# Performance work log

Measured on AMD Instinct MI355X. Metric: run time of the kernel, lower is better.

Reference implementation:

```python
import jax, jax.numpy as jnp
import numpy as np

B = 4096        # args.batch_size
M = 2           # n_views (and m in approximate_hsic_zy)
N = B * M       # total rows after torch.cat of views
D = 128         # projector feature dim
GAMMA = 3.0     # args.gamma
SIGMA = 1.0     # Gaussian kernel bandwidth used by compute_gaussian_kernel


def setup_inputs() -> dict:
    key = jax.random.key(0)
    x = jax.random.normal(key, (N, D), dtype=jnp.float32)
    # module applies l2_norm (F.normalize dim=1) before hsic_objective
    feat = x / jnp.maximum(jnp.linalg.norm(x, axis=1, keepdims=True), 1e-12)
    return {"feat": feat}


def _gaussian_kernel(x, y):
    # pairwise squared distances via the GEMM trick, then Gaussian kernel
    sq = (jnp.sum(x * x, axis=1)[:, None]
          + jnp.sum(y * y, axis=1)[None, :]
          - 2.0 * (x @ y.T))
    sq = jnp.maximum(sq, 0.0)
    return jnp.exp(-sq / (2.0 * SIGMA * SIGMA))


def _approximate_hsic_zy(K):
    # labels = cat([arange(B)]*M); labels-equality matrix; exclude diagonal.
    lab = jnp.tile(jnp.arange(B), M)                      # [N]
    eq = (lab[:, None] == lab[None, :]).astype(K.dtype)   # [N,N]
    offdiag = 1.0 - jnp.eye(N, dtype=K.dtype)
    # positives / negatives sums over off-diagonal entries (same math as the
    # boolean-mask view/reshape in torch, expressed as masked reductions)
    pos_sum = jnp.sum(K * eq * offdiag)
    neg_sum = jnp.sum(K * (1.0 - eq) * offdiag)
    term_1 = pos_sum / (B * M * (M - 1))
    term_2 = neg_sum / (B ** 2 * M ** 2)
    term_3 = 1.0 / (M - 1)
    scale = B / (B - 1.0)  # get_label_weights(batch_size) stand-in
    return scale * (term_1 - term_2 - term_3)


def _hsic_regular(K):
    # HSIC(z,z) with doubly-centered kernel: mean(Kc * Kc) since Kx == Ky
    row_m = jnp.mean(K, axis=0, keepdims=True)
    col_m = jnp.mean(K, axis=1, keepdims=True)
    tot_m = jnp.mean(K)
    Kc = K - row_m - col_m + tot_m
    return jnp.mean(Kc * Kc)


def reference(feat):
    K = _gaussian_kernel(feat, feat)          # [N,N] pairwise Gaussian kernel
    hsic_zy = _approximate_hsic_zy(K)
    hsic_zz = _hsic_regular(K)
    return -hsic_zy + GAMMA * jnp.sqrt(hsic_zz)
```

## Files before the change

kernel.cpp:

```cpp
#include <hip/hip_runtime.h>
#include <hip/hip_bf16.h>


using bf16   = __bf16;
using bf16x8 = __attribute__((ext_vector_type(8))) __bf16;
using f32x4  = __attribute__((ext_vector_type(4))) float;

#define N_ROWS 8192
#define LOG2E 1.4426950408889634f

#if __has_builtin(__builtin_amdgcn_exp2f)
#define EXP2(x) __builtin_amdgcn_exp2f(x)
#else
#define EXP2(x) exp2f(x)
#endif

__global__ __launch_bounds__(256) void prep_kernel(
    const float* __restrict__ feat, unsigned short* __restrict__ xb) {
  const int g = blockIdx.x * 256 + threadIdx.x;
  const float4 a = ((const float4*)feat)[g * 2];
  const float4 b = ((const float4*)feat)[g * 2 + 1];
  bf16x8 r;
  r[0] = (__bf16)a.x; r[1] = (__bf16)a.y; r[2] = (__bf16)a.z; r[3] = (__bf16)a.w;
  r[4] = (__bf16)b.x; r[5] = (__bf16)b.y; r[6] = (__bf16)b.z; r[7] = (__bf16)b.w;
  ((bf16x8*)xb)[g] = r;
}

__global__ __launch_bounds__(256, 2) void gram_kernel(
    const bf16* __restrict__ xb, float* __restrict__ rpart,
    float* __restrict__ bscal) {
  const int bjc = blockIdx.x, bi = blockIdx.y;
  const int tid = threadIdx.x, lane = tid & 63, w = tid >> 6;
  const int wr = w >> 1, wc = w & 1;
  const int l15 = lane & 15, l4 = lane >> 4;

  __shared__ char  lds_a[32768];
  __shared__ float rbuf[128];
  __shared__ float sS[4], sD[4], sP[4];

  {
    const int rowbase = bi * 128;
#pragma unroll
    for (int i = 0; i < 8; ++i) {
      const int c = tid + i * 256;
      const int row = c >> 4, seg = c & 15;
      const bf16x8 v = *(const bf16x8*)(xb + (rowbase + row) * 128 + seg * 8);
      const int sw = ((row << 8) | (seg << 4)) ^ ((row & 7) << 4);
      *(bf16x8*)(lds_a + sw) = v;
    }
    if (tid < 128) rbuf[tid] = 0.f;
  }
  __syncthreads();

  float rsum[4][4] = {};
  float s2a = 0.f, s2b = 0.f, pdiag = 0.f, ppos = 0.f;

  bf16x8 bn[4];
  {
    const int brow0 = (bjc * 4) * 128 + wc * 64;
#pragma unroll
    for (int f = 0; f < 4; ++f)
      bn[f] = *(const bf16x8*)(xb + (brow0 + f * 16 + l15) * 128 + l4 * 8);
  }

#pragma unroll
  for (int t = 0; t < 4; ++t) {
    const int bj = bjc * 4 + t;
    const int brow0 = bj * 128 + wc * 64;

    f32x4 acc[4][4];
#pragma unroll
    for (int fr = 0; fr < 4; ++fr)
#pragma unroll
      for (int fc = 0; fc < 4; ++fc)
#pragma unroll
        for (int e = 0; e < 4; ++e) acc[fr][fc][e] = -1.0f;

#pragma unroll
    for (int ks = 0; ks < 4; ++ks) {
      bf16x8 bb[4];
#pragma unroll
      for (int f = 0; f < 4; ++f) bb[f] = bn[f];

      if (ks < 3 || t < 3) {
        const int nks = (ks + 1) & 3;
        const int nbrow0 = (ks < 3) ? brow0 : brow0 + 128;
#pragma unroll
        for (int f = 0; f < 4; ++f)
          bn[f] = *(const bf16x8*)(xb + (nbrow0 + f * 16 + l15) * 128 +
                                   nks * 32 + l4 * 8);
      }

#pragma unroll
      for (int fr = 0; fr < 4; ++fr) {
        const int arow = wr * 64 + fr * 16 + l15;
        const int byte = (arow << 8) + ks * 64 + (l4 << 4);
        const bf16x8 a = *(const bf16x8*)(lds_a + (byte ^ ((arow & 7) << 4)));
#pragma unroll
        for (int fc = 0; fc < 4; ++fc)
          acc[fr][fc] = __builtin_amdgcn_mfma_f32_16x16x32_bf16(
              a, bb[fc], acc[fr][fc], 0, 0, 0);
      }
    }

    const int dt = bj - bi;
    const bool isd = (dt == 0);
    const bool isp = (dt == 32) | (dt == -32);

#pragma unroll
    for (int fr = 0; fr < 4; ++fr) {
#pragma unroll
      for (int fc = 0; fc < 4; ++fc) {
#pragma unroll
        for (int e = 0; e < 4; ++e) {
          const float me = fminf(acc[fr][fc][e], 0.f);
          const float K = EXP2(me * LOG2E);
          if (fc & 1) s2b = fmaf(K, K, s2b); else s2a = fmaf(K, K, s2a);
          rsum[fr][e] += K;
          if (isd | isp) {
            const int rr = wr * 64 + fr * 16 + l4 * 4 + e;
            const int cc = wc * 64 + fc * 16 + l15;
            const float hit = (rr == cc) ? K : 0.f;
            if (isd) pdiag += hit; else ppos += hit;
          }
        }
      }
    }
  }

#pragma unroll
  for (int fr = 0; fr < 4; ++fr) {
#pragma unroll
    for (int e = 0; e < 4; ++e) {
      float r = rsum[fr][e];
      r += __shfl_xor(r, 1);
      r += __shfl_xor(r, 2);
      r += __shfl_xor(r, 4);
      r += __shfl_xor(r, 8);
      if (l15 == 0) atomicAdd(&rbuf[wr * 64 + fr * 16 + l4 * 4 + e], r);
    }
  }
  float s2 = s2a + s2b;
#pragma unroll
  for (int m = 1; m < 64; m <<= 1) {
    s2 += __shfl_xor(s2, m);
    pdiag += __shfl_xor(pdiag, m);
    ppos += __shfl_xor(ppos, m);
  }
  if (lane == 0) { sS[w] = s2; sD[w] = pdiag; sP[w] = ppos; }
  __syncthreads();

  const int slot = bi * 16 + bjc;
  if (tid < 128) rpart[slot * 128 + tid] = rbuf[tid];
  if (tid == 0) {
    bscal[slot * 3 + 0] = sS[0] + sS[1] + sS[2] + sS[3];
    bscal[slot * 3 + 1] = sD[0] + sD[1] + sD[2] + sD[3];
    bscal[slot * 3 + 2] = sP[0] + sP[1] + sP[2] + sP[3];
  }
}

__global__ __launch_bounds__(256) void red1_kernel(
    const float* __restrict__ rpart, const float* __restrict__ bscal,
    double* __restrict__ gpart) {
  const int b = blockIdx.x, tid = threadIdx.x, lane = tid & 63, w = tid >> 6;
  double t = 0.0, v2 = 0.0, s2 = 0.0, dg = 0.0, ps = 0.0;
#pragma unroll
  for (int k = 0; k < 2; ++k) {
    const int row = b * 512 + k * 256 + tid;
    const int rb = row >> 7, r = row & 127;
    float s = 0.f;
#pragma unroll
    for (int c = 0; c < 16; ++c) s += rpart[(rb * 16 + c) * 128 + r];
    const double x = (double)s;
    t += x;
    v2 += x * x;
  }
  if (tid < 64) {
    const int i = b * 64 + tid;
    s2 = (double)bscal[i * 3 + 0];
    dg = (double)bscal[i * 3 + 1];
    ps = (double)bscal[i * 3 + 2];
  }
#pragma unroll
  for (int m = 1; m < 64; m <<= 1) {
    t += __shfl_xor(t, m);
    v2 += __shfl_xor(v2, m);
    s2 += __shfl_xor(s2, m);
    dg += __shfl_xor(dg, m);
    ps += __shfl_xor(ps, m);
  }
  __shared__ double sh[5][4];
  if (lane == 0) {
    sh[0][w] = t; sh[1][w] = v2; sh[2][w] = s2; sh[3][w] = dg; sh[4][w] = ps;
  }
  __syncthreads();
  if (tid == 0) {
    gpart[b * 5 + 0] = sh[0][0] + sh[0][1] + sh[0][2] + sh[0][3];
    gpart[b * 5 + 1] = sh[1][0] + sh[1][1] + sh[1][2] + sh[1][3];
    gpart[b * 5 + 2] = sh[2][0] + sh[2][1] + sh[2][2] + sh[2][3];
    gpart[b * 5 + 3] = sh[3][0] + sh[3][1] + sh[3][2] + sh[3][3];
    gpart[b * 5 + 4] = sh[4][0] + sh[4][1] + sh[4][2] + sh[4][3];
  }
}

__global__ __launch_bounds__(64) void red2_kernel(
    const double* __restrict__ gpart, float* __restrict__ out) {
  const int lane = threadIdx.x;
  double t = 0.0, v2 = 0.0, s2 = 0.0, dg = 0.0, ps = 0.0;
  if (lane < 16) {
    t  = gpart[lane * 5 + 0];
    v2 = gpart[lane * 5 + 1];
    s2 = gpart[lane * 5 + 2];
    dg = gpart[lane * 5 + 3];
    ps = gpart[lane * 5 + 4];
  }
#pragma unroll
  for (int m = 1; m < 16; m <<= 1) {
    t += __shfl_xor(t, m);
    v2 += __shfl_xor(v2, m);
    s2 += __shfl_xor(s2, m);
    dg += __shfl_xor(dg, m);
    ps += __shfl_xor(ps, m);
  }
  if (lane == 0) {
    const double Nd = 8192.0, Bd = 4096.0;
    const double hzz = (s2 - (2.0 / Nd) * v2 + (t * t) / (Nd * Nd)) / (Nd * Nd);
    const double neg = (t - dg) - ps;
    const double t1 = ps / 8192.0;
    const double t2 = neg / 67108864.0;
    const double hzy = (Bd / (Bd - 1.0)) * (t1 - t2 - 1.0);
    out[0] = (float)(-hzy + 3.0 * sqrt(fmax(hzz, 0.0)));
  }
}

extern "C" void kernel_launch(void* const* d_in, const int* in_sizes, int n_in,
                              void* d_out, int out_size, void* d_ws,
                              size_t ws_size, hipStream_t stream) {
  (void)in_sizes; (void)n_in; (void)out_size; (void)ws_size;
  const float* feat = (const float*)d_in[0];
  char* ws = (char*)d_ws;
  unsigned short* xb = (unsigned short*)ws;
  float* rpart  = (float*)(ws + 2097152);
  float* bscal  = (float*)(ws + 2097152 + 524288);
  double* gpart = (double*)(ws + 2097152 + 524288 + 12288);
  float* out = (float*)d_out;

  prep_kernel<<<512, 256, 0, stream>>>(feat, xb);
  gram_kernel<<<dim3(16, 64), 256, 0, stream>>>((const bf16*)xb, rpart, bscal);
  red1_kernel<<<16, 256, 0, stream>>>(rpart, bscal, gpart);
  red2_kernel<<<1, 64, 0, stream>>>(gpart, out);
}
```

Measured before the change: 138.9 us.

## Fuse reductions with last-block atomic counter and raise gram kernel occupancy

Merges the two reduction kernels into one 64-block kernel in which the last block to finish, found through an atomic counter that prep_kernel resets, computes the final scalar. This removes one kernel launch. The gram kernel's B-operand register prefetch and the unrolled outer tile loop are dropped in favour of direct per-step loads, and launch bounds rise to 4 blocks per SM. The intent is to cut register pressure and hide latency through occupancy instead of software prefetch, at the risk of exposed global-load latency and possible spills.

```diff
diff --git a/kernel.cpp b/kernel.cpp
--- a/kernel.cpp
+++ b/kernel.cpp
@@ -6,7 +6,6 @@
 using bf16x8 = __attribute__((ext_vector_type(8))) __bf16;
 using f32x4  = __attribute__((ext_vector_type(4))) float;
 
-#define N_ROWS 8192
 #define LOG2E 1.4426950408889634f
 
 #if __has_builtin(__builtin_amdgcn_exp2f)
@@ -16,7 +15,8 @@
 #endif
 
 __global__ __launch_bounds__(256) void prep_kernel(
-    const float* __restrict__ feat, unsigned short* __restrict__ xb) {
+    const float* __restrict__ feat, unsigned short* __restrict__ xb,
+    unsigned int* __restrict__ cnt) {
   const int g = blockIdx.x * 256 + threadIdx.x;
   const float4 a = ((const float4*)feat)[g * 2];
   const float4 b = ((const float4*)feat)[g * 2 + 1];
@@ -24,9 +24,10 @@
   r[0] = (__bf16)a.x; r[1] = (__bf16)a.y; r[2] = (__bf16)a.z; r[3] = (__bf16)a.w;
   r[4] = (__bf16)b.x; r[5] = (__bf16)b.y; r[6] = (__bf16)b.z; r[7] = (__bf16)b.w;
   ((bf16x8*)xb)[g] = r;
-}
-
-__global__ __launch_bounds__(256, 2) void gram_kernel(
+  if (blockIdx.x == 0 && threadIdx.x == 0) *cnt = 0u;
+}
+
+__global__ __launch_bounds__(256, 4) void gram_kernel(
     const bf16* __restrict__ xb, float* __restrict__ rpart,
     float* __restrict__ bscal) {
   const int bjc = blockIdx.x, bi = blockIdx.y;
@@ -55,15 +56,6 @@
   float rsum[4][4] = {};
   float s2a = 0.f, s2b = 0.f, pdiag = 0.f, ppos = 0.f;
 
-  bf16x8 bn[4];
-  {
-    const int brow0 = (bjc * 4) * 128 + wc * 64;
-#pragma unroll
-    for (int f = 0; f < 4; ++f)
-      bn[f] = *(const bf16x8*)(xb + (brow0 + f * 16 + l15) * 128 + l4 * 8);
-  }
-
-#pragma unroll
   for (int t = 0; t < 4; ++t) {
     const int bj = bjc * 4 + t;
     const int brow0 = bj * 128 + wc * 64;
@@ -80,17 +72,9 @@
     for (int ks = 0; ks < 4; ++ks) {
       bf16x8 bb[4];
 #pragma unroll
-      for (int f = 0; f < 4; ++f) bb[f] = bn[f];
-
-      if (ks < 3 || t < 3) {
-        const int nks = (ks + 1) & 3;
-        const int nbrow0 = (ks < 3) ? brow0 : brow0 + 128;
-#pragma unroll
-        for (int f = 0; f < 4; ++f)
-          bn[f] = *(const bf16x8*)(xb + (nbrow0 + f * 16 + l15) * 128 +
-                                   nks * 32 + l4 * 8);
-      }
-
+      for (int f = 0; f < 4; ++f)
+        bb[f] = *(const bf16x8*)(xb + (brow0 + f * 16 + l15) * 128 + ks * 32 +
+                                 l4 * 8);
 #pragma unroll
       for (int fr = 0; fr < 4; ++fr) {
         const int arow = wr * 64 + fr * 16 + l15;
@@ -159,24 +143,21 @@
   }
 }
 
-__global__ __launch_bounds__(256) void red1_kernel(
+__global__ __launch_bounds__(256) void red_kernel(
     const float* __restrict__ rpart, const float* __restrict__ bscal,
-    double* __restrict__ gpart) {
+    double* __restrict__ gpart, unsigned int* __restrict__ cnt,
+    float* __restrict__ out) {
   const int b = blockIdx.x, tid = threadIdx.x, lane = tid & 63, w = tid >> 6;
   double t = 0.0, v2 = 0.0, s2 = 0.0, dg = 0.0, ps = 0.0;
-#pragma unroll
-  for (int k = 0; k < 2; ++k) {
-    const int row = b * 512 + k * 256 + tid;
-    const int rb = row >> 7, r = row & 127;
+  if (tid < 128) {
     float s = 0.f;
 #pragma unroll
-    for (int c = 0; c < 16; ++c) s += rpart[(rb * 16 + c) * 128 + r];
-    const double x = (double)s;
-    t += x;
-    v2 += x * x;
-  }
-  if (tid < 64) {
-    const int i = b * 64 + tid;
+    for (int c = 0; c < 16; ++c) s += rpart[(b * 16 + c) * 128 + tid];
+    t = (double)s;
+    v2 = t * t;
+  }
+  if (tid < 16) {
+    const int i = b * 16 + tid;
     s2 = (double)bscal[i * 3 + 0];
     dg = (double)bscal[i * 3 + 1];
     ps = (double)bscal[i * 3 + 2];
@@ -190,6 +171,7 @@
     ps += __shfl_xor(ps, m);
   }
   __shared__ double sh[5][4];
+  __shared__ unsigned int sOld;
   if (lane == 0) {
     sh[0][w] = t; sh[1][w] = v2; sh[2][w] = s2; sh[3][w] = dg; sh[4][w] = ps;
   }
@@ -200,36 +182,37 @@
     gpart[b * 5 + 2] = sh[2][0] + sh[2][1] + sh[2][2] + sh[2][3];
     gpart[b * 5 + 3] = sh[3][0] + sh[3][1] + sh[3][2] + sh[3][3];
     gpart[b * 5 + 4] = sh[4][0] + sh[4][1] + sh[4][2] + sh[4][3];
-  }
-}
-
-__global__ __launch_bounds__(64) void red2_kernel(
-    const double* __restrict__ gpart, float* __restrict__ out) {
-  const int lane = threadIdx.x;
-  double t = 0.0, v2 = 0.0, s2 = 0.0, dg = 0.0, ps = 0.0;
-  if (lane < 16) {
-    t  = gpart[lane * 5 + 0];
-    v2 = gpart[lane * 5 + 1];
-    s2 = gpart[lane * 5 + 2];
-    dg = gpart[lane * 5 + 3];
-    ps = gpart[lane * 5 + 4];
-  }
-#pragma unroll
-  for (int m = 1; m < 16; m <<= 1) {
-    t += __shfl_xor(t, m);
-    v2 += __shfl_xor(v2, m);
-    s2 += __shfl_xor(s2, m);
-    dg += __shfl_xor(dg, m);
-    ps += __shfl_xor(ps, m);
-  }
-  if (lane == 0) {
-    const double Nd = 8192.0, Bd = 4096.0;
-    const double hzz = (s2 - (2.0 / Nd) * v2 + (t * t) / (Nd * Nd)) / (Nd * Nd);
-    const double neg = (t - dg) - ps;
-    const double t1 = ps / 8192.0;
-    const double t2 = neg / 67108864.0;
-    const double hzy = (Bd / (Bd - 1.0)) * (t1 - t2 - 1.0);
-    out[0] = (float)(-hzy + 3.0 * sqrt(fmax(hzz, 0.0)));
+    __threadfence();
+    sOld = atomicAdd(cnt, 1u);
+  }
+  __syncthreads();
+  if (sOld == 63u) {
+    __threadfence();
+    if (tid < 64) {
+      double ft = gpart[tid * 5 + 0];
+      double fv = gpart[tid * 5 + 1];
+      double fs = gpart[tid * 5 + 2];
+      double fd = gpart[tid * 5 + 3];
+      double fp = gpart[tid * 5 + 4];
+#pragma unroll
+      for (int m = 1; m < 64; m <<= 1) {
+        ft += __shfl_xor(ft, m);
+        fv += __shfl_xor(fv, m);
+        fs += __shfl_xor(fs, m);
+        fd += __shfl_xor(fd, m);
+        fp += __shfl_xor(fp, m);
+      }
+      if (tid == 0) {
+        const double Nd = 8192.0, Bd = 4096.0;
+        const double hzz =
+            (fs - (2.0 / Nd) * fv + (ft * ft) / (Nd * Nd)) / (Nd * Nd);
+        const double neg = (ft - fd) - fp;
+        const double t1 = fp / 8192.0;
+        const double t2 = neg / 67108864.0;
+        const double hzy = (Bd / (Bd - 1.0)) * (t1 - t2 - 1.0);
+        out[0] = (float)(-hzy + 3.0 * sqrt(fmax(hzz, 0.0)));
+      }
+    }
   }
 }
 
@@ -243,10 +226,10 @@
   float* rpart  = (float*)(ws + 2097152);
   float* bscal  = (float*)(ws + 2097152 + 524288);
   double* gpart = (double*)(ws + 2097152 + 524288 + 12288);
+  unsigned int* cnt = (unsigned int*)(ws + 2097152 + 524288 + 12288 + 2560);
   float* out = (float*)d_out;
 
-  prep_kernel<<<512, 256, 0, stream>>>(feat, xb);
+  prep_kernel<<<512, 256, 0, stream>>>(feat, xb, cnt);
   gram_kernel<<<dim3(16, 64), 256, 0, stream>>>((const bf16*)xb, rpart, bscal);
-  red1_kernel<<<16, 256, 0, stream>>>(rpart, bscal, gpart);
-  red2_kernel<<<1, 64, 0, stream>>>(gpart, out);
-}
+  red_kernel<<<64, 256, 0, stream>>>(rpart, bscal, gpart, cnt, (float*)d_out);
+}
```

New measurement: 172.0 us. 23.8% more time.
